# Kernel tuning notes

Hardware: AMD Instinct MI355X
Metric: run time of the kernel (lower is better)

The kernel has to match this reference:

```python
import jax, jax.numpy as jnp
import numpy as np

B, S, D = 4, 2048, 1024
H, DQ, DV = 16, 64, 64
LN_EPS = 1e-3  # keras LayerNormalization default


def _layer_norm(x, gamma, beta):
    mu = jnp.mean(x, axis=-1, keepdims=True)
    var = jnp.mean(jnp.square(x - mu), axis=-1, keepdims=True)
    return (x - mu) * jax.lax.rsqrt(var + LN_EPS) * gamma + beta


def setup_inputs() -> dict:
    key = jax.random.key(0)
    ks = jax.random.split(key, 6)
    x = jax.random.normal(ks[0], (B, S, D), jnp.float32)
    lengths = jax.random.randint(ks[1], (B,), 1, S + 1).astype(jnp.int32)
    scale = 0.02
    return {
        "query_sequences": x,
        "key_value_sequences": x,  # identical -> self-attention branch
        "key_value_sequence_lengths": lengths,
        "W_q": jax.random.normal(ks[2], (D, H * DQ), jnp.float32) * scale,
        "b_q": jnp.zeros((H * DQ,), jnp.float32),
        "W_kv": jax.random.normal(ks[3], (D, H * (DQ + DV)), jnp.float32) * scale,
        "b_kv": jnp.zeros((H * (DQ + DV),), jnp.float32),
        "W_o": jax.random.normal(ks[4], (H * DV, D), jnp.float32) * scale,
        "b_o": jnp.zeros((D,), jnp.float32),
        "ln_gamma": jnp.ones((D,), jnp.float32),
        "ln_beta": jnp.zeros((D,), jnp.float32),
    }


def reference(query_sequences, key_value_sequences, key_value_sequence_lengths,
              W_q, b_q, W_kv, b_kv, W_o, b_o, ln_gamma, ln_beta):
    # data-dependent self-attention detection, as in the TF code
    self_att = jnp.all(query_sequences == key_value_sequences)

    q_norm = _layer_norm(query_sequences, ln_gamma, ln_beta)
    kv_used = jnp.where(self_att, _layer_norm(key_value_sequences, ln_gamma, ln_beta),
                        key_value_sequences)
    residual = q_norm

    Q = (q_norm @ W_q + b_q).reshape(B, S, H, DQ)          # b q h d
    KV = kv_used @ W_kv + b_kv
    K = KV[..., : H * DQ].reshape(B, S, H, DQ)              # b k h d
    V = KV[..., H * DQ :].reshape(B, S, H, DV)              # b k h d

    scores = jnp.einsum("bqhd,bkhd->bhqk", Q, K) / np.sqrt(DQ).astype(np.float32)

    # key padding mask: key position < true length
    not_pad = (jnp.arange(S, dtype=jnp.int32)[None, None, None, :]
               < key_value_sequence_lengths[:, None, None, None])
    scores = jnp.where(not_pad, scores, -jnp.inf)
    # in_decoder=False -> no causal mask branch

    attn = jax.nn.softmax(scores, axis=-1)                  # dropout is identity at inference
    ctx = jnp.einsum("bhqk,bkhd->bqhd", attn, V).reshape(B, S, H * DV)
    out = ctx @ W_o + b_o + residual
    return out
```

## Files before the change

### kernel.cpp

```cpp
#include <hip/hip_runtime.h>
#include <hip/hip_bf16.h>
#include <cstdint>
#include <cmath>


#define DEV static __device__ __forceinline__

typedef float  f32x4 __attribute__((ext_vector_type(4)));
typedef short  s16x8 __attribute__((ext_vector_type(8)));
typedef short  s16x4 __attribute__((ext_vector_type(4)));
typedef __bf16 bf16x8 __attribute__((ext_vector_type(8)));
typedef unsigned int u32x4 __attribute__((ext_vector_type(4)));

DEV void gload_lds16(const void* g, void* l) {
  __builtin_amdgcn_global_load_lds(
      (const __attribute__((address_space(1))) unsigned int*)g,
      (__attribute__((address_space(3))) unsigned int*)l, 16, 0, 0);
}

DEV bf16x8 ldsv(const void* p) {
  return __builtin_bit_cast(bf16x8, *(const s16x8*)p);
}

DEV f32x4 mfma16(bf16x8 a, bf16x8 b, f32x4 c) {
  return __builtin_amdgcn_mfma_f32_16x16x32_bf16(a, b, c, 0, 0, 0);
}

DEV unsigned short f2b(float f) {
  __hip_bfloat16 h = __float2bfloat16(f);
  return __builtin_bit_cast(unsigned short, h);
}

DEV unsigned int cvt_pk_bf16(float lo, float hi) {
  unsigned int r;
  asm("v_cvt_pk_bf16_f32 %0, %1, %2" : "=v"(r) : "v"(lo), "v"(hi));
  return r;
}

#define MEMFENCE asm volatile("" ::: "memory")

__global__ __launch_bounds__(256) void ln_kernel(
    const float* __restrict__ x, const float* __restrict__ gamma,
    const float* __restrict__ beta, __hip_bfloat16* __restrict__ out)
{
  const int row = blockIdx.x, t = threadIdx.x;
  const float4 v = ((const float4*)(x + (size_t)row * 1024))[t];
  float s = v.x + v.y + v.z + v.w;
  float q = v.x * v.x + v.y * v.y + v.z * v.z + v.w * v.w;
#pragma unroll
  for (int m = 1; m < 64; m <<= 1) { s += __shfl_xor(s, m, 64); q += __shfl_xor(q, m, 64); }
  __shared__ float red[8];
  if ((t & 63) == 0) { red[t >> 6] = s; red[4 + (t >> 6)] = q; }
  __syncthreads();
  s = red[0] + red[1] + red[2] + red[3];
  q = red[4] + red[5] + red[6] + red[7];
  const float mu = s * (1.f / 1024.f);
  const float var = q * (1.f / 1024.f) - mu * mu;
  const float rs = rsqrtf(var + 1e-3f);
  const float4 g = ((const float4*)gamma)[t];
  const float4 bt = ((const float4*)beta)[t];
  s16x4 o;
  o[0] = (short)f2b((v.x - mu) * rs * g.x + bt.x);
  o[1] = (short)f2b((v.y - mu) * rs * g.y + bt.y);
  o[2] = (short)f2b((v.z - mu) * rs * g.z + bt.z);
  o[3] = (short)f2b((v.w - mu) * rs * g.w + bt.w);
  *(s16x4*)((short*)out + (size_t)row * 1024 + t * 4) = o;
}

__global__ __launch_bounds__(256) void wconv(
    const float* __restrict__ W, int N, __hip_bfloat16* __restrict__ Wt)
{
  __shared__ float tile[64][65];
  const int t = threadIdx.x;
  const int k0 = blockIdx.x * 64, n0 = blockIdx.y * 64;
#pragma unroll
  for (int p = 0; p < 4; ++p) {
    int r = p * 16 + (t >> 4), c4 = (t & 15) * 4;
    float4 v = *(const float4*)(W + (size_t)(k0 + r) * N + n0 + c4);
    tile[r][c4] = v.x; tile[r][c4 + 1] = v.y; tile[r][c4 + 2] = v.z; tile[r][c4 + 3] = v.w;
  }
  __syncthreads();
#pragma unroll
  for (int p = 0; p < 4; ++p) {
    int n = p * 16 + (t >> 4), kc = (t & 15) * 4;
    s16x4 o;
    o[0] = (short)f2b(tile[kc][n]);     o[1] = (short)f2b(tile[kc + 1][n]);
    o[2] = (short)f2b(tile[kc + 2][n]); o[3] = (short)f2b(tile[kc + 3][n]);
    *(s16x4*)((short*)Wt + (size_t)(n0 + n) * 1024 + k0 + kc) = o;
  }
}

__global__ __launch_bounds__(512, 2) void gemmP(
    const __hip_bfloat16* __restrict__ A, const __hip_bfloat16* __restrict__ Bt,
    const float* __restrict__ bias0, const float* __restrict__ bias1, int split,
    __hip_bfloat16* __restrict__ outb)
{
  __shared__ __align__(16) short sA[3 * 16384];
  __shared__ __align__(16) short sB[3 * 8192];
  const int t = threadIdx.x, l = t & 63, w = t >> 6;
  const int wr = w >> 1, wc = w & 1, lr = l & 15, lg = l >> 4;
  int bid = blockIdx.x;
  bid = (bid & 7) * 96 + (bid >> 3);
  const int bx = bid % 24, by = bid / 24;
  const int row0 = by * 256, col0 = bx * 128;
  const int NT = 16;

  f32x4 acc[4][4] = {};

  auto stageA2 = [&](int buf, int kt, int half) {
#pragma unroll
    for (int p = 0; p < 2; ++p) {
      const int L = (half * 2 + p) * 8192 + t * 16;
      const int r = L >> 7, c = (L >> 4) & 7;
      const int j = c ^ (r & 7);
      gload_lds16((const char*)A + ((size_t)(row0 + r) * 1024 + kt + j * 8) * 2,
                  (char*)sA + buf * 32768 + L);
    }
  };
  auto stageB1 = [&](int buf, int kt, int half) {
    const int L = half * 8192 + t * 16;
    const int r = L >> 7, c = (L >> 4) & 7;
    const int j = c ^ (r & 7);
    gload_lds16((const char*)Bt + ((size_t)(col0 + r) * 1024 + kt + j * 8) * 2,
                (char*)sB + buf * 16384 + L);
  };

  stageA2(0, 0, 0);  stageB1(0, 0, 0);  stageA2(0, 0, 1);  stageB1(0, 0, 1);
  stageA2(1, 64, 0); stageB1(1, 64, 0); stageA2(1, 64, 1); stageB1(1, 64, 1);
  asm volatile("s_waitcnt vmcnt(6)" ::: "memory");
  MEMFENCE; __builtin_amdgcn_s_barrier(); MEMFENCE;

#pragma unroll 1
  for (int ti = 0; ti < NT; ++ti) {
    const char* bA = (const char*)sA + (ti % 3) * 32768;
    const char* bB = (const char*)sB + (ti % 3) * 16384;
    const int nx = (ti + 2) % 3;
    const bool pre = (ti + 2 < NT);
#pragma unroll
    for (int kk = 0; kk < 2; ++kk) {
      bf16x8 af[4], bfr[4];
#pragma unroll
      for (int nb = 0; nb < 4; ++nb) {
        const int br = wc * 64 + nb * 16 + lr;
        bfr[nb] = ldsv(bB + br * 128 + (((kk * 4 + lg) ^ (br & 7)) * 16));
      }
#pragma unroll
      for (int mb = 0; mb < 4; ++mb) {
        const int ar = wr * 64 + mb * 16 + lr;
        af[mb] = ldsv(bA + ar * 128 + (((kk * 4 + lg) ^ (ar & 7)) * 16));
      }
      if (pre) { stageA2(nx, (ti + 2) * 64, kk); stageB1(nx, (ti + 2) * 64, kk); }
      MEMFENCE; __builtin_amdgcn_s_barrier(); MEMFENCE;
      asm volatile("s_waitcnt lgkmcnt(0)" ::: "memory");
      __builtin_amdgcn_s_setprio(1);
#pragma unroll
      for (int mb = 0; mb < 4; ++mb)
#pragma unroll
        for (int nb = 0; nb < 4; ++nb)
          acc[mb][nb] = mfma16(af[mb], bfr[nb], acc[mb][nb]);
      __builtin_amdgcn_s_setprio(0);
      if (kk == 1) {
        if (pre) asm volatile("s_waitcnt vmcnt(6)" ::: "memory");
        else     asm volatile("s_waitcnt vmcnt(0)" ::: "memory");
      }
      MEMFENCE; __builtin_amdgcn_s_barrier(); MEMFENCE;
    }
  }

#pragma unroll
  for (int mb = 0; mb < 4; ++mb) {
    const int rbase = row0 + wr * 64 + mb * 16 + lg * 4;
#pragma unroll
    for (int nb = 0; nb < 4; ++nb) {
      const int col = col0 + wc * 64 + nb * 16 + lr;
      const float bias = (col < split) ? bias0[col] : bias1[col - split];
#pragma unroll
      for (int jr = 0; jr < 4; ++jr)
        outb[(size_t)(rbase + jr) * 3072 + col] = __float2bfloat16(acc[mb][nb][jr] + bias);
    }
  }
}

__global__ __launch_bounds__(256, 2) void gemm_bt(
    const __hip_bfloat16* __restrict__ A, const __hip_bfloat16* __restrict__ Bt,
    const float* __restrict__ bias0,
    const __hip_bfloat16* __restrict__ resid, float* __restrict__ outf)
{
  __shared__ __align__(16) short sA[128 * 64];
  __shared__ __align__(16) short sB[128 * 64];
  const int t = threadIdx.x, l = t & 63, w = t >> 6;
  const int wr = w >> 1, wc = w & 1, lr = l & 15, lg = l >> 4;
  const int row0 = blockIdx.y * 128, col0 = blockIdx.x * 128;
  f32x4 acc[4][4] = {};

  for (int kt = 0; kt < 1024; kt += 64) {
#pragma unroll
    for (int p = 0; p < 4; ++p) {
      const int L = p * 4096 + t * 16;
      const int r = L >> 7, c = ((L >> 4) & 7) ^ (r & 7);
      gload_lds16((const char*)A + ((size_t)(row0 + r) * 1024 + kt + c * 8) * 2, (char*)sA + L);
    }
#pragma unroll
    for (int p = 0; p < 4; ++p) {
      const int L = p * 4096 + t * 16;
      const int r = L >> 7, c = ((L >> 4) & 7) ^ (r & 7);
      gload_lds16((const char*)Bt + ((size_t)(col0 + r) * 1024 + kt + c * 8) * 2, (char*)sB + L);
    }
    __syncthreads();

    bf16x8 af[4][2], bfr[4][2];
#pragma unroll
    for (int mb = 0; mb < 4; ++mb) {
      const int ar = wr * 64 + mb * 16 + lr;
#pragma unroll
      for (int kk = 0; kk < 2; ++kk)
        af[mb][kk] = ldsv((const char*)sA + ar * 128 + (((kk * 4 + lg) ^ (ar & 7)) * 16));
    }
#pragma unroll
    for (int nb = 0; nb < 4; ++nb) {
      const int br = wc * 64 + nb * 16 + lr;
#pragma unroll
      for (int kk = 0; kk < 2; ++kk)
        bfr[nb][kk] = ldsv((const char*)sB + br * 128 + (((kk * 4 + lg) ^ (br & 7)) * 16));
    }
#pragma unroll
    for (int kk = 0; kk < 2; ++kk)
#pragma unroll
      for (int mb = 0; mb < 4; ++mb)
#pragma unroll
        for (int nb = 0; nb < 4; ++nb)
          acc[mb][nb] = mfma16(af[mb][kk], bfr[nb][kk], acc[mb][nb]);
    __syncthreads();
  }

#pragma unroll
  for (int mb = 0; mb < 4; ++mb) {
    const int rbase = row0 + wr * 64 + mb * 16 + lg * 4;
#pragma unroll
    for (int nb = 0; nb < 4; ++nb) {
      const int col = col0 + wc * 64 + nb * 16 + lr;
      const float bias = bias0[col];
#pragma unroll
      for (int jr = 0; jr < 4; ++jr) {
        const size_t idx = (size_t)(rbase + jr) * 1024 + col;
        outf[idx] = acc[mb][nb][jr] + bias + __bfloat162float(resid[idx]);
      }
    }
  }
}

__global__ __launch_bounds__(256) void vtrans(
    const __hip_bfloat16* __restrict__ qkv, __hip_bfloat16* __restrict__ vt)
{
  __shared__ __align__(16) short tile[64][72];
  const int t = threadIdx.x;
  const int s0 = blockIdx.x * 64;
  const int bh = blockIdx.y, b = bh >> 4, h = bh & 15;
#pragma unroll
  for (int p = 0; p < 2; ++p) {
    int idx = p * 256 + t;
    int r = idx >> 3, c = idx & 7;
    s16x8 vv = *(const s16x8*)((const short*)qkv +
        (size_t)(b * 2048 + s0 + r) * 3072 + 2048 + h * 64 + c * 8);
    *(s16x8*)((char*)tile + r * 144 + c * 16) = vv;
  }
  __syncthreads();
  const int dv = t >> 2, sc = (t & 3) * 16;
  s16x8 a, bvec;
#pragma unroll
  for (int e = 0; e < 8; ++e) a[e] = tile[sc + e][dv];
#pragma unroll
  for (int e = 0; e < 8; ++e) bvec[e] = tile[sc + 8 + e][dv];
  short* dst = (short*)vt + (size_t)(bh * 64 + dv) * 2048 + s0 + sc;
  *(s16x8*)dst = a;
  *(s16x8*)(dst + 8) = bvec;
}

__global__ __launch_bounds__(256, 4) void attn_kernel(
    const __hip_bfloat16* __restrict__ qkv, const __hip_bfloat16* __restrict__ vt,
    const int* __restrict__ lens, __hip_bfloat16* __restrict__ ctx)
{
  __shared__ __align__(16) short sK[2][64 * 64];
  __shared__ __align__(16) short sV[2][64 * 64];
  const int t = threadIdx.x, l = t & 63, w = t >> 6;
  const int lr = l & 15, lg = l >> 4;
  const int bh = blockIdx.y, b = bh >> 4, h = bh & 15;
  const int q0 = blockIdx.x * 128 + w * 32;
  const int len = lens[b];
  const float NEG = -__builtin_inff();
  const float QSC = 0.18033688f;

  bf16x8 qf[2][2];
#pragma unroll
  for (int mbt = 0; mbt < 2; ++mbt)
#pragma unroll
    for (int kk = 0; kk < 2; ++kk) {
      bf16x8 r = ldsv((const char*)qkv +
          ((size_t)(b * 2048 + q0 + mbt * 16 + lr) * 3072 + h * 64 + kk * 32 + lg * 8) * 2);
#pragma unroll
      for (int e = 0; e < 8; ++e) qf[mbt][kk][e] = (__bf16)((float)r[e] * QSC);
    }

  f32x4 o[4][2] = {};
  float mrun[2] = {NEG, NEG}, ssum[2] = {0.f, 0.f};

  auto stage = [&](short* dK, short* dV, int kv0) {
#pragma unroll
    for (int p = 0; p < 2; ++p) {
      const int L = p * 4096 + t * 16;
      const int r = L >> 7, c = ((L >> 4) & 7) ^ (r & 7);
      gload_lds16((const char*)qkv +
          ((size_t)(b * 2048 + kv0 + r) * 3072 + 1024 + h * 64 + c * 8) * 2, (char*)dK + L);
    }
#pragma unroll
    for (int p = 0; p < 2; ++p) {
      const int L = p * 4096 + t * 16;
      const int r = L >> 7, c = ((L >> 4) & 7) ^ (r & 7);
      gload_lds16((const char*)vt +
          ((size_t)(bh * 64 + r) * 2048 + kv0 + c * 8) * 2, (char*)dV + L);
    }
  };

  const int nt = (len + 63) >> 6;
  short* curK = sK[0]; short* nxtK = sK[1];
  short* curV = sV[0]; short* nxtV = sV[1];
  stage(curK, curV, 0);

  const int srcA = (lg & 1) * 32 + lr;
  const int srcB = srcA + 16;

  for (int ti = 0; ti < nt; ++ti) {
    const int kv0 = ti * 64;
    if (ti + 1 < nt) {
      stage(nxtK, nxtV, kv0 + 64);
      asm volatile("s_waitcnt vmcnt(4)" ::: "memory");
    } else {
      asm volatile("s_waitcnt vmcnt(0)" ::: "memory");
    }
    MEMFENCE; __builtin_amdgcn_s_barrier(); MEMFENCE;

    f32x4 sf[2][4] = {};
    __builtin_amdgcn_s_setprio(1);
#pragma unroll
    for (int kk = 0; kk < 2; ++kk) {
      bf16x8 ak[4];
#pragma unroll
      for (int nbt = 0; nbt < 4; ++nbt) {
        const int br = nbt * 16 + lr;
        ak[nbt] = ldsv((const char*)curK + br * 128 + (((kk * 4 + lg) ^ (br & 7)) * 16));
      }
#pragma unroll
      for (int mbt = 0; mbt < 2; ++mbt)
#pragma unroll
        for (int nbt = 0; nbt < 4; ++nbt)
          sf[mbt][nbt] = mfma16(ak[nbt], qf[mbt][kk], sf[mbt][nbt]);
    }
    __builtin_amdgcn_s_setprio(0);

    if (kv0 + 64 > len) {
#pragma unroll
      for (int nbt = 0; nbt < 4; ++nbt)
#pragma unroll
        for (int jr = 0; jr < 4; ++jr)
          if (kv0 + nbt * 16 + lg * 4 + jr >= len) {
            sf[0][nbt][jr] = NEG;
            sf[1][nbt][jr] = NEG;
          }
    }

    float rm[2];
#pragma unroll
    for (int mbt = 0; mbt < 2; ++mbt) {
      f32x4 m4 = sf[mbt][0];
      m4 = __builtin_elementwise_max(m4, sf[mbt][1]);
      m4 = __builtin_elementwise_max(m4, sf[mbt][2]);
      m4 = __builtin_elementwise_max(m4, sf[mbt][3]);
      float m0 = fmaxf(fmaxf(m4[0], m4[1]), fmaxf(m4[2], m4[3]));
      m0 = fmaxf(m0, __shfl_xor(m0, 16, 64));
      m0 = fmaxf(m0, __shfl_xor(m0, 32, 64));
      rm[mbt] = m0;
    }
    const bool need = (rm[0] > mrun[0] + 3.f) || (rm[1] > mrun[1] + 3.f);
    if (__any(need)) {
#pragma unroll
      for (int mbt = 0; mbt < 2; ++mbt) {
        const float mnew = fmaxf(mrun[mbt], rm[mbt]);
        const float corr = __builtin_amdgcn_exp2f(mrun[mbt] - mnew);
        mrun[mbt] = mnew;
        ssum[mbt] *= corr;
#pragma unroll
        for (int nbt2 = 0; nbt2 < 4; ++nbt2) o[nbt2][mbt] *= corr;
      }
    }
    unsigned int W0[2][4], W1[2][4];
#pragma unroll
    for (int mbt = 0; mbt < 2; ++mbt) {
      f32x4 ts = {0.f, 0.f, 0.f, 0.f};
#pragma unroll
      for (int nbt = 0; nbt < 4; ++nbt) {
        f32x4 pe;
#pragma unroll
        for (int jr = 0; jr < 4; ++jr)
          pe[jr] = __builtin_amdgcn_exp2f(sf[mbt][nbt][jr] - mrun[mbt]);
        ts += pe;
        W0[mbt][nbt] = cvt_pk_bf16(pe[0], pe[1]);
        W1[mbt][nbt] = cvt_pk_bf16(pe[2], pe[3]);
      }
      ssum[mbt] += (ts[0] + ts[1]) + (ts[2] + ts[3]);
    }

#pragma unroll
    for (int c = 0; c < 2; ++c) {
      bf16x8 vf[4], pb[2];
#pragma unroll
      for (int nbt2 = 0; nbt2 < 4; ++nbt2) {
        const int vr = nbt2 * 16 + lr;
        vf[nbt2] = ldsv((const char*)curV + vr * 128 + (((c * 4 + lg) ^ (vr & 7)) * 16));
      }
#pragma unroll
      for (int mbt = 0; mbt < 2; ++mbt) {
        const unsigned int selW0 = (lg & 2) ? W0[mbt][2 * c + 1] : W0[mbt][2 * c];
        const unsigned int selW1 = (lg & 2) ? W1[mbt][2 * c + 1] : W1[mbt][2 * c];
        u32x4 bw;
        bw[0] = __shfl((int)selW0, srcA, 64);
        bw[1] = __shfl((int)selW1, srcA, 64);
        bw[2] = __shfl((int)selW0, srcB, 64);
        bw[3] = __shfl((int)selW1, srcB, 64);
        pb[mbt] = __builtin_bit_cast(bf16x8, bw);
      }
      __builtin_amdgcn_s_setprio(1);
#pragma unroll
      for (int nbt2 = 0; nbt2 < 4; ++nbt2)
#pragma unroll
        for (int mbt = 0; mbt < 2; ++mbt)
          o[nbt2][mbt] = mfma16(vf[nbt2], pb[mbt], o[nbt2][mbt]);
      __builtin_amdgcn_s_setprio(0);
    }

    asm volatile("s_waitcnt lgkmcnt(0)" ::: "memory");
    MEMFENCE; __builtin_amdgcn_s_barrier(); MEMFENCE;
    short* tk = curK; curK = nxtK; nxtK = tk;
    short* tv = curV; curV = nxtV; nxtV = tv;
  }

  float inv[2];
#pragma unroll
  for (int mbt = 0; mbt < 2; ++mbt) {
    float s = ssum[mbt];
    s += __shfl_xor(s, 16, 64);
    s += __shfl_xor(s, 32, 64);
    inv[mbt] = 1.f / s;
  }
  char* eb = (char*)sK + w * 4352;
#pragma unroll
  for (int mbt = 0; mbt < 2; ++mbt)
#pragma unroll
    for (int nbt2 = 0; nbt2 < 4; ++nbt2)
#pragma unroll
      for (int jr = 0; jr < 4; ++jr)
        *(short*)(eb + (mbt * 16 + lr) * 136 + (nbt2 * 16 + lg * 4 + jr) * 2) =
            (short)f2b(o[nbt2][mbt][jr] * inv[mbt]);
  asm volatile("s_waitcnt lgkmcnt(0)" ::: "memory");
  __builtin_amdgcn_sched_barrier(0);
  const int qi = l >> 1, half = l & 1;
#pragma unroll
  for (int i = 0; i < 4; ++i) {
    s16x8 v = *(const s16x8*)(eb + qi * 136 + half * 64 + i * 16);
    *(s16x8*)((short*)ctx + (size_t)(b * 2048 + q0 + qi) * 1024 + h * 64 + half * 32 + i * 8) = v;
  }
}

extern "C" void kernel_launch(void* const* d_in, const int* in_sizes, int n_in,
                              void* d_out, int out_size, void* d_ws, size_t ws_size,
                              hipStream_t stream)
{
  const float* x     = (const float*)d_in[0];
  const int*   lens  = (const int*)d_in[2];
  const float* Wq    = (const float*)d_in[3];
  const float* bq    = (const float*)d_in[4];
  const float* Wkv   = (const float*)d_in[5];
  const float* bkv   = (const float*)d_in[6];
  const float* Wo    = (const float*)d_in[7];
  const float* bo    = (const float*)d_in[8];
  const float* gamma = (const float*)d_in[9];
  const float* beta  = (const float*)d_in[10];
  float* out = (float*)d_out;

  char* ws = (char*)d_ws;
  __hip_bfloat16* ln  = (__hip_bfloat16*)(ws);
  __hip_bfloat16* qkv = (__hip_bfloat16*)(ws + ((size_t)16 << 20));
  __hip_bfloat16* vt  = (__hip_bfloat16*)(ws + ((size_t)64 << 20));
  __hip_bfloat16* ctx = (__hip_bfloat16*)(ws + ((size_t)80 << 20));
  __hip_bfloat16* wt  = (__hip_bfloat16*)(ws + ((size_t)96 << 20));
  __hip_bfloat16* wot = (__hip_bfloat16*)(ws + ((size_t)102 << 20));

  ln_kernel<<<dim3(8192), dim3(256), 0, stream>>>(x, gamma, beta, ln);
  wconv<<<dim3(16, 16), dim3(256), 0, stream>>>(Wq, 1024, wt);
  wconv<<<dim3(16, 32), dim3(256), 0, stream>>>(Wkv, 2048, wt + (size_t)1024 * 1024);
  wconv<<<dim3(16, 16), dim3(256), 0, stream>>>(Wo, 1024, wot);
  gemmP<<<dim3(768), dim3(512), 0, stream>>>(ln, wt, bq, bkv, 1024, qkv);
  vtrans<<<dim3(32, 64), dim3(256), 0, stream>>>(qkv, vt);
  attn_kernel<<<dim3(16, 64), dim3(256), 0, stream>>>(qkv, vt, lens, ctx);
  gemm_bt<<<dim3(8, 64), dim3(256), 0, stream>>>(ctx, wot, bo, ln, out);
}
```

Measured before the change: 181.1 us.

## Replace pipelined 256x128 QKV GEMM with simple single-buffered 128x128 kernel

Swaps the triple-buffered, 512-thread QKV projection GEMM for a simpler 256-thread kernel with 128x128 tiles and one LDS buffer per operand, synchronising twice per k-step. It launches twice as many blocks, with smaller LDS use and possibly higher occupancy. The cost is losing the overlap of global-to-LDS loads with MFMA compute and reusing each loaded A tile less. Kernels are also renamed and the split constant is hardcoded.

```diff
diff --git a/kernel.cpp b/kernel.cpp
--- a/kernel.cpp
+++ b/kernel.cpp
@@ -90,81 +90,59 @@
   }
 }
 
-__global__ __launch_bounds__(512, 2) void gemmP(
+__global__ __launch_bounds__(256, 2) void gemm_qkv(
     const __hip_bfloat16* __restrict__ A, const __hip_bfloat16* __restrict__ Bt,
-    const float* __restrict__ bias0, const float* __restrict__ bias1, int split,
+    const float* __restrict__ bias0, const float* __restrict__ bias1,
     __hip_bfloat16* __restrict__ outb)
 {
-  __shared__ __align__(16) short sA[3 * 16384];
-  __shared__ __align__(16) short sB[3 * 8192];
+  __shared__ __align__(16) short sA[128 * 64];
+  __shared__ __align__(16) short sB[128 * 64];
   const int t = threadIdx.x, l = t & 63, w = t >> 6;
   const int wr = w >> 1, wc = w & 1, lr = l & 15, lg = l >> 4;
-  int bid = blockIdx.x;
-  bid = (bid & 7) * 96 + (bid >> 3);
-  const int bx = bid % 24, by = bid / 24;
-  const int row0 = by * 256, col0 = bx * 128;
-  const int NT = 16;
-
+  int lin = (int)blockIdx.x;
+  lin = (lin & 7) * 192 + (lin >> 3);
+  const int bx = lin % 24, by = lin / 24;
+  const int row0 = by * 128, col0 = bx * 128;
   f32x4 acc[4][4] = {};
 
-  auto stageA2 = [&](int buf, int kt, int half) {
-#pragma unroll
-    for (int p = 0; p < 2; ++p) {
-      const int L = (half * 2 + p) * 8192 + t * 16;
-      const int r = L >> 7, c = (L >> 4) & 7;
-      const int j = c ^ (r & 7);
-      gload_lds16((const char*)A + ((size_t)(row0 + r) * 1024 + kt + j * 8) * 2,
-                  (char*)sA + buf * 32768 + L);
-    }
-  };
-  auto stageB1 = [&](int buf, int kt, int half) {
-    const int L = half * 8192 + t * 16;
-    const int r = L >> 7, c = (L >> 4) & 7;
-    const int j = c ^ (r & 7);
-    gload_lds16((const char*)Bt + ((size_t)(col0 + r) * 1024 + kt + j * 8) * 2,
-                (char*)sB + buf * 16384 + L);
-  };
-
-  stageA2(0, 0, 0);  stageB1(0, 0, 0);  stageA2(0, 0, 1);  stageB1(0, 0, 1);
-  stageA2(1, 64, 0); stageB1(1, 64, 0); stageA2(1, 64, 1); stageB1(1, 64, 1);
-  asm volatile("s_waitcnt vmcnt(6)" ::: "memory");
-  MEMFENCE; __builtin_amdgcn_s_barrier(); MEMFENCE;
-
-#pragma unroll 1
-  for (int ti = 0; ti < NT; ++ti) {
-    const char* bA = (const char*)sA + (ti % 3) * 32768;
-    const char* bB = (const char*)sB + (ti % 3) * 16384;
-    const int nx = (ti + 2) % 3;
-    const bool pre = (ti + 2 < NT);
-#pragma unroll
-    for (int kk = 0; kk < 2; ++kk) {
-      bf16x8 af[4], bfr[4];
-#pragma unroll
-      for (int nb = 0; nb < 4; ++nb) {
-        const int br = wc * 64 + nb * 16 + lr;
-        bfr[nb] = ldsv(bB + br * 128 + (((kk * 4 + lg) ^ (br & 7)) * 16));
-      }
-#pragma unroll
-      for (int mb = 0; mb < 4; ++mb) {
-        const int ar = wr * 64 + mb * 16 + lr;
-        af[mb] = ldsv(bA + ar * 128 + (((kk * 4 + lg) ^ (ar & 7)) * 16));
-      }
-      if (pre) { stageA2(nx, (ti + 2) * 64, kk); stageB1(nx, (ti + 2) * 64, kk); }
-      MEMFENCE; __builtin_amdgcn_s_barrier(); MEMFENCE;
-      asm volatile("s_waitcnt lgkmcnt(0)" ::: "memory");
-      __builtin_amdgcn_s_setprio(1);
+  for (int kt = 0; kt < 1024; kt += 64) {
+#pragma unroll
+    for (int p = 0; p < 4; ++p) {
+      const int L = p * 4096 + t * 16;
+      const int r = L >> 7, c = ((L >> 4) & 7) ^ (r & 7);
+      gload_lds16((const char*)A + ((size_t)(row0 + r) * 1024 + kt + c * 8) * 2, (char*)sA + L);
+    }
+#pragma unroll
+    for (int p = 0; p < 4; ++p) {
+      const int L = p * 4096 + t * 16;
+      const int r = L >> 7, c = ((L >> 4) & 7) ^ (r & 7);
+      gload_lds16((const char*)Bt + ((size_t)(col0 + r) * 1024 + kt + c * 8) * 2, (char*)sB + L);
+    }
+    __syncthreads();
+
+    bf16x8 af[4][2], bfr[4][2];
+#pragma unroll
+    for (int mb = 0; mb < 4; ++mb) {
+      const int ar = wr * 64 + mb * 16 + lr;
+#pragma unroll
+      for (int kk = 0; kk < 2; ++kk)
+        af[mb][kk] = ldsv((const char*)sA + ar * 128 + (((kk * 4 + lg) ^ (ar & 7)) * 16));
+    }
+#pragma unroll
+    for (int nb = 0; nb < 4; ++nb) {
+      const int br = wc * 64 + nb * 16 + lr;
+#pragma unroll
+      for (int kk = 0; kk < 2; ++kk)
+        bfr[nb][kk] = ldsv((const char*)sB + br * 128 + (((kk * 4 + lg) ^ (br & 7)) * 16));
+    }
+#pragma unroll
+    for (int kk = 0; kk < 2; ++kk)
 #pragma unroll
       for (int mb = 0; mb < 4; ++mb)
 #pragma unroll
         for (int nb = 0; nb < 4; ++nb)
-          acc[mb][nb] = mfma16(af[mb], bfr[nb], acc[mb][nb]);
-      __builtin_amdgcn_s_setprio(0);
-      if (kk == 1) {
-        if (pre) asm volatile("s_waitcnt vmcnt(6)" ::: "memory");
-        else     asm volatile("s_waitcnt vmcnt(0)" ::: "memory");
-      }
-      MEMFENCE; __builtin_amdgcn_s_barrier(); MEMFENCE;
-    }
+          acc[mb][nb] = mfma16(af[mb][kk], bfr[nb][kk], acc[mb][nb]);
+    __syncthreads();
   }
 
 #pragma unroll
@@ -173,7 +151,7 @@
 #pragma unroll
     for (int nb = 0; nb < 4; ++nb) {
       const int col = col0 + wc * 64 + nb * 16 + lr;
-      const float bias = (col < split) ? bias0[col] : bias1[col - split];
+      const float bias = (col < 1024) ? bias0[col] : bias1[col - 1024];
 #pragma unroll
       for (int jr = 0; jr < 4; ++jr)
         outb[(size_t)(rbase + jr) * 3072 + col] = __float2bfloat16(acc[mb][nb][jr] + bias);
@@ -181,7 +159,7 @@
   }
 }
 
-__global__ __launch_bounds__(256, 2) void gemm_bt(
+__global__ __launch_bounds__(256, 2) void gemm_out(
     const __hip_bfloat16* __restrict__ A, const __hip_bfloat16* __restrict__ Bt,
     const float* __restrict__ bias0,
     const __hip_bfloat16* __restrict__ resid, float* __restrict__ outf)
@@ -498,8 +476,8 @@
   wconv<<<dim3(16, 16), dim3(256), 0, stream>>>(Wq, 1024, wt);
   wconv<<<dim3(16, 32), dim3(256), 0, stream>>>(Wkv, 2048, wt + (size_t)1024 * 1024);
   wconv<<<dim3(16, 16), dim3(256), 0, stream>>>(Wo, 1024, wot);
-  gemmP<<<dim3(768), dim3(512), 0, stream>>>(ln, wt, bq, bkv, 1024, qkv);
+  gemm_qkv<<<dim3(1536), dim3(256), 0, stream>>>(ln, wt, bq, bkv, qkv);
   vtrans<<<dim3(32, 64), dim3(256), 0, stream>>>(qkv, vt);
   attn_kernel<<<dim3(16, 64), dim3(256), 0, stream>>>(qkv, vt, lens, ctx);
-  gemm_bt<<<dim3(8, 64), dim3(256), 0, stream>>>(ctx, wot, bo, ln, out);
-}
+  gemm_out<<<dim3(8, 64), dim3(256), 0, stream>>>(ctx, wot, bo, ln, out);
+}
```

After: 175.7 us. 1.03x faster.
